# Performance work log

Measured on AMD Instinct MI355X. Metric: run time of the kernel, lower is better.

The kernel has to match this reference:

```python
import jax, jax.numpy as jnp
import numpy as np

B, T, NODES, D = 8, 32, 400, 64   # batch graphs, time steps, stocks, node_feat_dim==lstm_dim
N = B * T * NODES                 # 102400 total nodes
E = 1_638_400                     # edges (avg degree 16)
L1, L2, FC1, FC2 = 96, 64, 128, 3

def setup_inputs() -> dict:
    key = jax.random.key(0)
    ks = jax.random.split(key, 12)
    rn = lambda k, shape, s=0.05: jax.random.normal(k, shape, jnp.float32) * s
    return {
        "x": jax.random.normal(ks[0], (N, D), jnp.float32),
        "edge_attr": jax.random.normal(ks[1], (E, 2), jnp.float32),
        "conv1_w": rn(ks[2], (D, L1)), "conv1_b": jnp.zeros((L1,), jnp.float32),
        "conv2_w": rn(ks[3], (L1, L2)), "conv2_b": jnp.zeros((L2,), jnp.float32),
        "lstm_w_ih": rn(ks[4], (4 * D, D)), "lstm_w_hh": rn(ks[5], (4 * D, D)),
        "lstm_b_ih": jnp.zeros((4 * D,), jnp.float32), "lstm_b_hh": jnp.zeros((4 * D,), jnp.float32),
        "fc1_w": rn(ks[6], (FC1, L2)), "fc1_b": jnp.zeros((FC1,), jnp.float32),
        "fc2_w": rn(ks[7], (FC2, FC1)), "fc2_b": jnp.zeros((FC2,), jnp.float32),
        "edge_index": jax.random.randint(ks[8], (2, E), 0, N, jnp.int32),
    }

def _normalize(x):
    m = x.mean(axis=0, keepdims=True)
    s = x.std(axis=0, ddof=1, keepdims=True)  # torch.std uses ddof=1
    return (x - m) / s

def _gcn(x, W, b, src, dst, ew):
    """GCNConv with edge weights: add self-loops (weight 1), symmetric norm, scatter-add."""
    n = x.shape[0]
    loops = jnp.arange(n, dtype=src.dtype)
    src2 = jnp.concatenate([src, loops])
    dst2 = jnp.concatenate([dst, loops])
    ew2 = jnp.concatenate([ew, jnp.ones((n,), ew.dtype)])
    deg = jax.ops.segment_sum(ew2, dst2, num_segments=n)
    dis = jnp.where(deg > 0, jax.lax.rsqrt(jnp.where(deg > 0, deg, 1.0)), 0.0)
    norm = dis[src2] * ew2 * dis[dst2]
    h = x @ W                                        # [N, out]
    return jax.ops.segment_sum(h[src2] * norm[:, None], dst2, num_segments=n) + b

def _lstm_last(xseq, w_ih, w_hh, b_ih, b_hh):
    """Single-layer LSTM (torch gate order i,f,g,o); returns last hidden state."""
    Bn = xseq.shape[0]
    H = w_hh.shape[1]
    xg = jnp.einsum('btd,gd->tbg', xseq, w_ih) + (b_ih + b_hh)  # [T, Bn, 4H]
    def step(carry, g_in):
        h, c = carry
        g = g_in + h @ w_hh.T
        i, f, gg, o = jnp.split(g, 4, axis=-1)
        c = jax.nn.sigmoid(f) * c + jax.nn.sigmoid(i) * jnp.tanh(gg)
        h = jax.nn.sigmoid(o) * jnp.tanh(c)
        return (h, c), None
    init = (jnp.zeros((Bn, H), xseq.dtype), jnp.zeros((Bn, H), xseq.dtype))
    (h, _), _ = jax.lax.scan(step, init, xg)
    return h

def reference(x, edge_attr, conv1_w, conv1_b, conv2_w, conv2_b,
              lstm_w_ih, lstm_w_hh, lstm_b_ih, lstm_b_hh,
              fc1_w, fc1_b, fc2_w, fc2_b, edge_index):
    xn = _normalize(x)
    ew = jnp.abs(edge_attr[:, 0])        # args.edgetype = 0
    src, dst = edge_index[0], edge_index[1]
    # (first LSTM over raw x in the original is dead code: output immediately overwritten)
    h = jax.nn.relu(_gcn(xn, conv1_w, conv1_b, src, dst, ew))
    h = jax.nn.relu(_gcn(h, conv2_w, conv2_b, src, dst, ew))
    # to_dense_batch (batch-contiguous nodes) + reshape/permute into per-node time series
    h = h.reshape(B, T, NODES, L2).transpose(0, 2, 1, 3).reshape(B * NODES, T, L2)
    h = _lstm_last(h, lstm_w_ih, lstm_w_hh, lstm_b_ih, lstm_b_hh)   # [B*NODES, L2]
    h = jax.nn.relu(h @ fc1_w.T + fc1_b)
    logits = h @ fc2_w.T + fc2_b
    p = jax.nn.softmax(logits, axis=1)   # softmax over class dim of 2D tensor
    return p.reshape(B, NODES, FC2)
```

## Files before the change

kernel.cpp:

```cpp
#include <hip/hip_runtime.h>
#include <hip/hip_bf16.h>
#include <hip/hip_fp16.h>

#define NN 102400
#define DD 64
#define EE 1638400
#define L1C 96
#define L2C 64
#define TT 32
#define NODESC 400
#define BB 8
#define SS 3200
#define G4 256

#define NBUK 400
#define BCAP 5120
#define PCHUNK 2048
#define NPART (EE / PCHUNK)
#define PTHR 512
#define EPT (PCHUNK / PTHR)

#define OFF_ENT  ((size_t)0)
#define OFF_A1   ((size_t)4096000)
#define OFF_G1   ((size_t)10649600)
#define OFF_ENT2 ((size_t)26214400)
#define OFF_H2   ((size_t)26214400)
#define OFF_G2   ((size_t)32768000)
#define OFF_GCUR ((size_t)39321600)
#define OFF_DIS  ((size_t)39328000)
#define OFF_RNG  ((size_t)39430400)
#define OFF_HL   ((size_t)39635200)
#define OFF_ST   ((size_t)39840000)

typedef __attribute__((ext_vector_type(8))) _Float16 f16x8;
typedef __attribute__((ext_vector_type(4))) float f32x4;

__device__ __forceinline__ void fma4(float4& a, float s, const float4& w) {
    a.x = fmaf(s, w.x, a.x); a.y = fmaf(s, w.y, a.y);
    a.z = fmaf(s, w.z, a.z); a.w = fmaf(s, w.w, a.w);
}
__device__ __forceinline__ float rcp_f(float x) { return __builtin_amdgcn_rcpf(x); }
__device__ __forceinline__ float sigm_f(float x) {
    x = fminf(fmaxf(x, -30.f), 30.f);
    return rcp_f(1.f + __expf(-x));
}
__device__ __forceinline__ float tanh_f(float x) {
    x = fminf(fmaxf(x, -15.f), 15.f);
    float e = __expf(2.f * x);
    return (e - 1.f) * rcp_f(e + 1.f);
}
__device__ __forceinline__ unsigned short f32_bf16_rtne(float f) {
    unsigned int u = __float_as_uint(f);
    unsigned int r = u + 0x7fffu + ((u >> 16) & 1u);
    return (unsigned short)(r >> 16);
}
__device__ __forceinline__ float bf16_f32(unsigned short h) {
    return __uint_as_float(((unsigned int)h) << 16);
}
__device__ __forceinline__ float4 unp4(uint2 p) {
    float4 v;
    v.x = __uint_as_float(p.x << 16);
    v.y = __uint_as_float(p.x & 0xffff0000u);
    v.z = __uint_as_float(p.y << 16);
    v.w = __uint_as_float(p.y & 0xffff0000u);
    return v;
}
__device__ __forceinline__ uint2 pk4(float4 v) {
    unsigned int u0 = ((unsigned int)f32_bf16_rtne(v.y) << 16) | f32_bf16_rtne(v.x);
    unsigned int u1 = ((unsigned int)f32_bf16_rtne(v.w) << 16) | f32_bf16_rtne(v.z);
    return make_uint2(u0, u1);
}
__device__ __forceinline__ uint2 pkh4(float4 v) {
    __half2 h0 = __floats2half2_rn(v.x, v.y);
    __half2 h1 = __floats2half2_rn(v.z, v.w);
    uint2 r;
    r.x = *(unsigned int*)&h0;
    r.y = *(unsigned int*)&h1;
    return r;
}
__device__ __forceinline__ float4 uph4(uint2 p) {
    __half2 h0 = *(__half2*)&p.x;
    __half2 h1 = *(__half2*)&p.y;
    float2 f0 = __half22float2(h0), f1 = __half22float2(h1);
    return make_float4(f0.x, f0.y, f1.x, f1.y);
}

__global__ void init_zero(int* gcur, float* st) {
    int idx = blockIdx.x * 256 + threadIdx.x;
    if (idx < NBUK * 16) gcur[idx] = 0;
    if (blockIdx.x == 0 && threadIdx.x < 128) st[threadIdx.x] = 0.f;
}

__global__ __launch_bounds__(256) void col_sums(const float* __restrict__ x, float* __restrict__ st) {
    int c = threadIdx.x & 63;
    size_t i = (size_t)blockIdx.x * 256 + threadIdx.x;
    size_t stride = (size_t)gridDim.x * 256;
    float s = 0.f, q = 0.f;
    for (size_t e = i; e < (size_t)NN * 64; e += stride) {
        float v = x[e]; s += v; q = fmaf(v, v, q);
    }
    __shared__ float ls[128];
    if (threadIdx.x < 128) ls[threadIdx.x] = 0.f;
    __syncthreads();
    atomicAdd(&ls[c], s); atomicAdd(&ls[64 + c], q);
    __syncthreads();
    if (threadIdx.x < 128) atomicAdd(&st[threadIdx.x], ls[threadIdx.x]);
}

__global__ void finalize_stats(float* st) {
    int c = threadIdx.x;
    if (c < 64) {
        float s = st[c], q = st[64 + c];
        float mean = s / (float)NN;
        float var = (q - s * s / (float)NN) / (float)(NN - 1);
        st[128 + c] = mean;
        st[192 + c] = rsqrtf(fmaxf(var, 1e-20f));
    }
}

__global__ __launch_bounds__(256) void xnd_kernel(const float* __restrict__ x, const float* __restrict__ st,
                                                  const float* __restrict__ dis, uint2* __restrict__ xnd) {
    size_t i = (size_t)blockIdx.x * 256 + threadIdx.x;
    int n = (int)(i >> 4), q = (int)(i & 15);
    float4 v = ((const float4*)x)[i];
    float4 mean4 = ((const float4*)(st + 128))[q];
    float4 istd4 = ((const float4*)(st + 192))[q];
    float dn = dis[n];
    v.x = (v.x - mean4.x) * istd4.x * dn;
    v.y = (v.y - mean4.y) * istd4.y * dn;
    v.z = (v.z - mean4.z) * istd4.z * dn;
    v.w = (v.w - mean4.w) * istd4.w * dn;
    xnd[i] = pk4(v);
}

__global__ __launch_bounds__(PTHR) void part_kernel(const int* __restrict__ ei, const float* __restrict__ ea,
                                                    int* __restrict__ gcur, int2* __restrict__ ent2) {
    __shared__ int lhist[NBUK];
    __shared__ int lofs[NBUK];
    __shared__ int lbase[NBUK];
    __shared__ int scn[PTHR];
    __shared__ int2 stage[PCHUNK];
    __shared__ int  gdst[PCHUNK];
    const int tid = threadIdx.x;
    const int e0 = blockIdx.x * PCHUNK;
    for (int i = tid; i < NBUK; i += PTHR) lhist[i] = 0;
    __syncthreads();
    int   dv[EPT]; int sv[EPT]; float wvv[EPT];
    #pragma unroll
    for (int i = 0; i < EPT; ++i) {
        int e = e0 + i * PTHR + tid;
        dv[i]  = ei[EE + e];
        sv[i]  = ei[e];
        wvv[i] = fabsf(ea[2 * (size_t)e]);
        atomicAdd(&lhist[dv[i] >> 8], 1);
    }
    __syncthreads();
    scn[tid] = (tid < NBUK) ? lhist[tid] : 0;
    __syncthreads();
    for (int d = 1; d < PTHR; d <<= 1) {
        int t = (tid >= d) ? scn[tid - d] : 0;
        __syncthreads();
        scn[tid] += t;
        __syncthreads();
    }
    if (tid < NBUK) {
        lofs[tid]  = scn[tid] - lhist[tid];
        lbase[tid] = atomicAdd(&gcur[tid * 16], lhist[tid]);
        lhist[tid] = 0;
    }
    __syncthreads();
    #pragma unroll
    for (int i = 0; i < EPT; ++i) {
        int d = dv[i];
        int b = d >> 8;
        int li = atomicAdd(&lhist[b], 1);
        int pos = lofs[b] + li;
        stage[pos] = make_int2(sv[i] | ((d & 255) << 24), __float_as_int(wvv[i]));
        int gp_ = lbase[b] + li;
        gdst[pos] = (gp_ < BCAP) ? (b * BCAP + gp_) : -1;
    }
    __syncthreads();
    for (int i = tid; i < PCHUNK; i += PTHR) {
        int g = gdst[i];
        if (g >= 0) ent2[g] = stage[i];
    }
}

__global__ __launch_bounds__(256) void bucket_csr(const int2* __restrict__ ent2, const int* __restrict__ gcur,
                                                  int2* __restrict__ ent, int2* __restrict__ rng,
                                                  float* __restrict__ dis) {
    __shared__ int nhist[256];
    __shared__ int scn[256];
    __shared__ float wsum[256];
    __shared__ int pcur[256];
    const int tid = threadIdx.x;
    const int b = blockIdx.x;
    const int base = b * BCAP;
    int cnt = gcur[b * 16];
    if (cnt > BCAP) cnt = BCAP;
    nhist[tid] = 0;
    wsum[tid] = 0.f;
    __syncthreads();
    for (int e = tid; e < cnt; e += 256) {
        int2 en = ent2[base + e];
        int dl = ((unsigned)en.x) >> 24;
        atomicAdd(&nhist[dl], 1);
        atomicAdd(&wsum[dl], __int_as_float(en.y));
    }
    __syncthreads();
    int c = nhist[tid];
    scn[tid] = c;
    __syncthreads();
    for (int d = 1; d < 256; d <<= 1) {
        int t = (tid >= d) ? scn[tid - d] : 0;
        __syncthreads();
        scn[tid] += t;
        __syncthreads();
    }
    int ps = scn[tid] - c;
    rng[b * 256 + tid] = make_int2(base + ps, base + ps + c);
    dis[b * 256 + tid] = rsqrtf(1.f + wsum[tid]);
    pcur[tid] = ps;
    __syncthreads();
    for (int e = tid; e < cnt; e += 256) {
        int2 en = ent2[base + e];
        int dl = ((unsigned)en.x) >> 24;
        int local = atomicAdd(&pcur[dl], 1);
        ent[base + local] = make_int2(en.x & 0xFFFFFF, en.y);
    }
}

template<int K, int NC, int MB, int THREADS, bool PRELU, bool DISO, bool HIN, bool HOUT>
__global__ __launch_bounds__(THREADS) void gemm_tiled(
    const float* __restrict__ A, const float* __restrict__ Wm,
    const float* __restrict__ bin, const float* __restrict__ dscale,
    float* __restrict__ Cm, int ldC)
{
    __shared__ float As[MB * K];
    __shared__ float Ws[K * NC];

    for (int i = threadIdx.x; i < K * NC / 4; i += THREADS)
        ((float4*)Ws)[i] = ((const float4*)Wm)[i];

    size_t row0 = (size_t)blockIdx.x * MB;
    for (int i = threadIdx.x; i < MB * (K / 4); i += THREADS) {
        int r = i / (K / 4); int c = (i % (K / 4)) * 4;
        float4 a;
        if (HIN) {
            uint2 p = *(const uint2*)((const unsigned short*)A + (row0 + r) * K + c);
            a = uph4(p);
        } else {
            a = *(const float4*)(A + (row0 + r) * K + c);
        }
        if (PRELU) {
            a.x = fmaxf(a.x + bin[c + 0], 0.f); a.y = fmaxf(a.y + bin[c + 1], 0.f);
            a.z = fmaxf(a.z + bin[c + 2], 0.f); a.w = fmaxf(a.w + bin[c + 3], 0.f);
        }
        ((float4*)As)[i] = a;
    }
    __syncthreads();

    constexpr int NCT = NC / 4;
    int tc = threadIdx.x % NCT;
    int tr = threadIdx.x / NCT;
    int r = tr * 4;
    float4 acc[4];
    acc[0] = acc[1] = acc[2] = acc[3] = make_float4(0.f, 0.f, 0.f, 0.f);

    #pragma unroll 8
    for (int d4 = 0; d4 < K / 4; ++d4) {
        float4 w0 = ((const float4*)Ws)[(4 * d4 + 0) * NCT + tc];
        float4 w1 = ((const float4*)Ws)[(4 * d4 + 1) * NCT + tc];
        float4 w2 = ((const float4*)Ws)[(4 * d4 + 2) * NCT + tc];
        float4 w3 = ((const float4*)Ws)[(4 * d4 + 3) * NCT + tc];
        #pragma unroll
        for (int i = 0; i < 4; ++i) {
            float4 av = ((const float4*)As)[(r + i) * (K / 4) + d4];
            fma4(acc[i], av.x, w0); fma4(acc[i], av.y, w1);
            fma4(acc[i], av.z, w2); fma4(acc[i], av.w, w3);
        }
    }

    #pragma unroll
    for (int i = 0; i < 4; ++i) {
        size_t row = row0 + r + i;
        float4 o = acc[i];
        if (DISO) {
            float dn = dscale[row];
            o.x *= dn; o.y *= dn; o.z *= dn; o.w *= dn;
            *(uint2*)((unsigned short*)Cm + row * ldC + tc * 4) = pk4(o);
        } else if (HOUT) {
            *(uint2*)((unsigned short*)Cm + row * ldC + tc * 4) = pkh4(o);
        } else {
            *(float4*)(Cm + row * ldC + tc * 4) = o;
        }
    }
}

template<int C4>
__global__ __launch_bounds__(256) void gcn_gather(const uint2* __restrict__ h, const int2* __restrict__ rng,
                                                  const int2* __restrict__ ent, const float* __restrict__ dis,
                                                  unsigned short* __restrict__ g) {
    unsigned int idx = blockIdx.x * 256 + threadIdx.x;
    unsigned int n = idx / C4, q = idx % C4;
    float4 acc = unp4(h[(size_t)n * C4 + q]);
    int2 r = rng[n];
    int e = r.x;
    for (; e + 8 <= r.y; e += 8) {
        int2 en0 = ent[e],     en1 = ent[e + 1], en2 = ent[e + 2], en3 = ent[e + 3];
        int2 en4 = ent[e + 4], en5 = ent[e + 5], en6 = ent[e + 6], en7 = ent[e + 7];
        uint2 v0 = h[(size_t)en0.x * C4 + q];
        uint2 v1 = h[(size_t)en1.x * C4 + q];
        uint2 v2 = h[(size_t)en2.x * C4 + q];
        uint2 v3 = h[(size_t)en3.x * C4 + q];
        uint2 v4 = h[(size_t)en4.x * C4 + q];
        uint2 v5 = h[(size_t)en5.x * C4 + q];
        uint2 v6 = h[(size_t)en6.x * C4 + q];
        uint2 v7 = h[(size_t)en7.x * C4 + q];
        fma4(acc, __int_as_float(en0.y), unp4(v0));
        fma4(acc, __int_as_float(en1.y), unp4(v1));
        fma4(acc, __int_as_float(en2.y), unp4(v2));
        fma4(acc, __int_as_float(en3.y), unp4(v3));
        fma4(acc, __int_as_float(en4.y), unp4(v4));
        fma4(acc, __int_as_float(en5.y), unp4(v5));
        fma4(acc, __int_as_float(en6.y), unp4(v6));
        fma4(acc, __int_as_float(en7.y), unp4(v7));
    }
    for (; e + 4 <= r.y; e += 4) {
        int2 en0 = ent[e], en1 = ent[e + 1], en2 = ent[e + 2], en3 = ent[e + 3];
        uint2 v0 = h[(size_t)en0.x * C4 + q];
        uint2 v1 = h[(size_t)en1.x * C4 + q];
        uint2 v2 = h[(size_t)en2.x * C4 + q];
        uint2 v3 = h[(size_t)en3.x * C4 + q];
        fma4(acc, __int_as_float(en0.y), unp4(v0));
        fma4(acc, __int_as_float(en1.y), unp4(v1));
        fma4(acc, __int_as_float(en2.y), unp4(v2));
        fma4(acc, __int_as_float(en3.y), unp4(v3));
    }
    for (; e < r.y; ++e) {
        int2 en = ent[e];
        uint2 v = h[(size_t)en.x * C4 + q];
        fma4(acc, __int_as_float(en.y), unp4(v));
    }
    float dn = dis[n];
    acc.x *= dn; acc.y *= dn; acc.z *= dn; acc.w *= dn;
    *(uint2*)(g + (size_t)n * (C4 * 4) + q * 4) = pkh4(acc);
}

#define XP_LD 72
#define HP_LD2 72
#define GP_LD 258

__global__ __launch_bounds__(512, 1) void lstm_kernel(
    const __half* __restrict__ g2, const float* __restrict__ cb2,
    const float* __restrict__ whh, const float* __restrict__ wih,
    const float* __restrict__ bih, const float* __restrict__ bhh,
    float* __restrict__ hlast)
{
    __shared__ __align__(16) _Float16 xpack[32 * 16 * XP_LD];
    __shared__ __align__(16) _Float16 hhi[16 * HP_LD2];
    __shared__ __align__(16) _Float16 hlo[16 * HP_LD2];
    __shared__ float gp[16 * GP_LD];
    const int tid  = threadIdx.x;
    const int lane = tid & 63;
    const int wv   = tid >> 6;
    const int n15  = lane & 15;
    const int quad = lane >> 4;
    const int ja   = lane;

    f16x8 whh_h[2][2], whh_l[2][2], wih_h[2][2], wih_l[2][2];
    #pragma unroll
    for (int tl = 0; tl < 2; ++tl) {
        const int gate = (wv + 8 * tl) * 16 + n15;
        const float* wp = whh + (size_t)gate * 64 + quad * 8;
        const float* xp = wih + (size_t)gate * 64 + quad * 8;
        #pragma unroll
        for (int kc = 0; kc < 2; ++kc) {
            #pragma unroll
            for (int j = 0; j < 8; ++j) {
                float w = wp[kc * 32 + j];
                _Float16 h = (_Float16)w;
                whh_h[tl][kc][j] = h;
                whh_l[tl][kc][j] = (_Float16)((w - (float)h) * 2048.f);
                float v = xp[kc * 32 + j];
                _Float16 g = (_Float16)v;
                wih_h[tl][kc][j] = g;
                wih_l[tl][kc][j] = (_Float16)((v - (float)g) * 2048.f);
            }
        }
    }

    const float bi_i = bih[ja]        + bhh[ja];
    const float bi_f = bih[64 + ja]   + bhh[64 + ja];
    const float bi_g = bih[128 + ja]  + bhh[128 + ja];
    const float bi_o = bih[192 + ja]  + bhh[192 + ja];

    {
        const int s0 = blockIdx.x * 16;
        const int b_ = s0 / NODESC;
        const int node0 = s0 - b_ * NODESC;
        const int r  = (tid >> 4) & 15;
        const int c4 = tid & 15;
        const int t0 = tid >> 8;
        float4 bias4 = *(const float4*)(cb2 + c4 * 4);
        _Float16* dst = xpack + r * XP_LD + c4 * 4;
        const __half* src = g2 + ((size_t)(b_ * TT + t0) * NODESC + node0 + r) * 64 + c4 * 4;
        #pragma unroll
        for (int i = 0; i < 16; ++i) {
            uint2 p = *(const uint2*)(src + (size_t)i * 2 * NODESC * 64);
            float4 v = uph4(p);
            v.x = fmaxf(v.x + bias4.x, 0.f);
            v.y = fmaxf(v.y + bias4.y, 0.f);
            v.z = fmaxf(v.z + bias4.z, 0.f);
            v.w = fmaxf(v.w + bias4.w, 0.f);
            *(uint2*)(dst + (size_t)(t0 + i * 2) * (16 * XP_LD)) = pkh4(v);
        }
    }

    for (int i = tid; i < 16 * HP_LD2; i += 512) { hhi[i] = (_Float16)0.f; hlo[i] = (_Float16)0.f; }
    float cA_reg = 0.f, hA = 0.f;
    float cB_reg = 0.f, hB = 0.f;
    __syncthreads();

    const int xbase = n15 * XP_LD + quad * 8;
    const int hbase = n15 * HP_LD2 + quad * 8;

    for (int t = 0; t < TT; ++t) {
        f32x4 cmA  = {0.f,0.f,0.f,0.f}, clA0 = {0.f,0.f,0.f,0.f}, clA1 = {0.f,0.f,0.f,0.f};
        f32x4 cmB  = {0.f,0.f,0.f,0.f}, clB0 = {0.f,0.f,0.f,0.f}, clB1 = {0.f,0.f,0.f,0.f};
        const _Float16* xrow = xpack + (size_t)t * (16 * XP_LD);
        {
            f16x8 ax0 = *(const f16x8*)(xrow + xbase);
            f16x8 ah0 = *(const f16x8*)(hhi + hbase);
            f16x8 al0 = *(const f16x8*)(hlo + hbase);
            f16x8 ax1 = *(const f16x8*)(xrow + xbase + 32);
            f16x8 ah1 = *(const f16x8*)(hhi + hbase + 32);
            f16x8 al1 = *(const f16x8*)(hlo + hbase + 32);
            cmA  = __builtin_amdgcn_mfma_f32_16x16x32_f16(ax0, wih_h[0][0], cmA,  0, 0, 0);
            cmB  = __builtin_amdgcn_mfma_f32_16x16x32_f16(ax0, wih_h[1][0], cmB,  0, 0, 0);
            clA0 = __builtin_amdgcn_mfma_f32_16x16x32_f16(ax0, wih_l[0][0], clA0, 0, 0, 0);
            clB0 = __builtin_amdgcn_mfma_f32_16x16x32_f16(ax0, wih_l[1][0], clB0, 0, 0, 0);
            clA1 = __builtin_amdgcn_mfma_f32_16x16x32_f16(ax1, wih_l[0][1], clA1, 0, 0, 0);
            clB1 = __builtin_amdgcn_mfma_f32_16x16x32_f16(ax1, wih_l[1][1], clB1, 0, 0, 0);
            cmA  = __builtin_amdgcn_mfma_f32_16x16x32_f16(ah0, whh_h[0][0], cmA,  0, 0, 0);
            cmB  = __builtin_amdgcn_mfma_f32_16x16x32_f16(ah0, whh_h[1][0], cmB,  0, 0, 0);
            clA0 = __builtin_amdgcn_mfma_f32_16x16x32_f16(al0, whh_h[0][0], clA0, 0, 0, 0);
            clB0 = __builtin_amdgcn_mfma_f32_16x16x32_f16(al0, whh_h[1][0], clB0, 0, 0, 0);
            clA1 = __builtin_amdgcn_mfma_f32_16x16x32_f16(al1, whh_h[0][1], clA1, 0, 0, 0);
            clB1 = __builtin_amdgcn_mfma_f32_16x16x32_f16(al1, whh_h[1][1], clB1, 0, 0, 0);
            cmA  = __builtin_amdgcn_mfma_f32_16x16x32_f16(ax1, wih_h[0][1], cmA,  0, 0, 0);
            cmB  = __builtin_amdgcn_mfma_f32_16x16x32_f16(ax1, wih_h[1][1], cmB,  0, 0, 0);
            clA0 = __builtin_amdgcn_mfma_f32_16x16x32_f16(ah0, whh_l[0][0], clA0, 0, 0, 0);
            clB0 = __builtin_amdgcn_mfma_f32_16x16x32_f16(ah0, whh_l[1][0], clB0, 0, 0, 0);
            clA1 = __builtin_amdgcn_mfma_f32_16x16x32_f16(ah1, whh_l[0][1], clA1, 0, 0, 0);
            clB1 = __builtin_amdgcn_mfma_f32_16x16x32_f16(ah1, whh_l[1][1], clB1, 0, 0, 0);
            cmA  = __builtin_amdgcn_mfma_f32_16x16x32_f16(ah1, whh_h[0][1], cmA,  0, 0, 0);
            cmB  = __builtin_amdgcn_mfma_f32_16x16x32_f16(ah1, whh_h[1][1], cmB,  0, 0, 0);
        }
        f32x4 cA = cmA + (clA0 + clA1) * (1.f / 2048.f);
        f32x4 cB = cmB + (clB0 + clB1) * (1.f / 2048.f);
        #pragma unroll
        for (int r = 0; r < 4; ++r) {
            gp[(quad * 4 + r) * GP_LD + wv * 16 + n15]       = cA[r];
            gp[(quad * 4 + r) * GP_LD + (wv + 8) * 16 + n15] = cB[r];
        }
        __syncthreads();

        {
            const int qa = wv;
            float gi = gp[qa * GP_LD + ja]        + bi_i;
            float gf = gp[qa * GP_LD + 64 + ja]   + bi_f;
            float gg = gp[qa * GP_LD + 128 + ja]  + bi_g;
            float go = gp[qa * GP_LD + 192 + ja]  + bi_o;
            cA_reg = sigm_f(gf) * cA_reg + sigm_f(gi) * tanh_f(gg);
            hA = sigm_f(go) * tanh_f(cA_reg);
            _Float16 hh = (_Float16)hA;
            hhi[qa * HP_LD2 + ja] = hh;
            hlo[qa * HP_LD2 + ja] = (_Float16)((hA - (float)hh) * 2048.f);
        }
        {
            const int qa = wv + 8;
            float gi = gp[qa * GP_LD + ja]        + bi_i;
            float gf = gp[qa * GP_LD + 64 + ja]   + bi_f;
            float gg = gp[qa * GP_LD + 128 + ja]  + bi_g;
            float go = gp[qa * GP_LD + 192 + ja]  + bi_o;
            cB_reg = sigm_f(gf) * cB_reg + sigm_f(gi) * tanh_f(gg);
            hB = sigm_f(go) * tanh_f(cB_reg);
            _Float16 hh = (_Float16)hB;
            hhi[qa * HP_LD2 + ja] = hh;
            hlo[qa * HP_LD2 + ja] = (_Float16)((hB - (float)hh) * 2048.f);
        }
        __syncthreads();
    }
    hlast[((size_t)blockIdx.x * 16 + wv) * 64 + ja]     = hA;
    hlast[((size_t)blockIdx.x * 16 + wv + 8) * 64 + ja] = hB;
}

__global__ __launch_bounds__(128) void head_kernel(const float* __restrict__ hl,
                                                   const float* __restrict__ w1, const float* __restrict__ b1,
                                                   const float* __restrict__ w2, const float* __restrict__ b2,
                                                   float* __restrict__ out) {
    __shared__ float hrow[64];
    __shared__ float a1[128];
    __shared__ float lg[3];
    int s = blockIdx.x, tid = threadIdx.x;
    if (tid < 64) hrow[tid] = hl[(size_t)s * 64 + tid];
    __syncthreads();
    {
        const float4* wr = (const float4*)(w1 + (size_t)tid * 64);
        const float4* hq = (const float4*)hrow;
        float4 acc = make_float4(0.f, 0.f, 0.f, 0.f);
        #pragma unroll
        for (int k = 0; k < 16; ++k) {
            float4 wv = wr[k]; float4 hv = hq[k];
            acc.x = fmaf(wv.x, hv.x, acc.x); acc.y = fmaf(wv.y, hv.y, acc.y);
            acc.z = fmaf(wv.z, hv.z, acc.z); acc.w = fmaf(wv.w, hv.w, acc.w);
        }
        a1[tid] = fmaxf((acc.x + acc.y) + (acc.z + acc.w) + b1[tid], 0.f);
    }
    __syncthreads();
    if (tid < 3) {
        const float4* wr = (const float4*)(w2 + (size_t)tid * 128);
        const float4* aq = (const float4*)a1;
        float4 acc = make_float4(0.f, 0.f, 0.f, 0.f);
        #pragma unroll
        for (int k = 0; k < 32; ++k) {
            float4 wv = wr[k]; float4 av = aq[k];
            acc.x = fmaf(wv.x, av.x, acc.x); acc.y = fmaf(wv.y, av.y, acc.y);
            acc.z = fmaf(wv.z, av.z, acc.z); acc.w = fmaf(wv.w, av.w, acc.w);
        }
        lg[tid] = (acc.x + acc.y) + (acc.z + acc.w) + b2[tid];
    }
    __syncthreads();
    if (tid == 0) {
        float m = fmaxf(lg[0], fmaxf(lg[1], lg[2]));
        float e0 = __expf(lg[0] - m), e1 = __expf(lg[1] - m), e2 = __expf(lg[2] - m);
        float inv = 1.f / (e0 + e1 + e2);
        out[(size_t)s * 3 + 0] = e0 * inv;
        out[(size_t)s * 3 + 1] = e1 * inv;
        out[(size_t)s * 3 + 2] = e2 * inv;
    }
}

extern "C" void kernel_launch(void* const* d_in, const int* in_sizes, int n_in,
                              void* d_out, int out_size, void* d_ws, size_t ws_size,
                              hipStream_t stream) {
    (void)in_sizes; (void)n_in; (void)out_size; (void)ws_size;
    const float* x        = (const float*)d_in[0];
    const float* ea       = (const float*)d_in[1];
    const float* conv1_w  = (const float*)d_in[2];
    const float* conv1_b  = (const float*)d_in[3];
    const float* conv2_w  = (const float*)d_in[4];
    const float* conv2_b  = (const float*)d_in[5];
    const float* w_ih     = (const float*)d_in[6];
    const float* w_hh     = (const float*)d_in[7];
    const float* b_ih     = (const float*)d_in[8];
    const float* b_hh     = (const float*)d_in[9];
    const float* fc1_w    = (const float*)d_in[10];
    const float* fc1_b    = (const float*)d_in[11];
    const float* fc2_w    = (const float*)d_in[12];
    const float* fc2_b    = (const float*)d_in[13];
    const int*   ei       = (const int*)d_in[14];
    float* out = (float*)d_out;

    float* W    = (float*)d_ws;
    int2*  ent  = (int2*)(W + OFF_ENT);
    unsigned short* a1h = (unsigned short*)(W + OFF_A1);
    unsigned short* g1h = (unsigned short*)(W + OFF_G1);
    int2*  ent2 = (int2*)(W + OFF_ENT2);
    uint2* xnd  = (uint2*)(W + OFF_ENT2);
    float* h2   = W + OFF_H2;
    unsigned short* g2h = (unsigned short*)(W + OFF_G2);
    int*   gcur = (int*)(W + OFF_GCUR);
    float* dis  = W + OFF_DIS;
    int2*  rng  = (int2*)(W + OFF_RNG);
    float* hl   = W + OFF_HL;
    float* st   = W + OFF_ST;

    init_zero<<<26, 256, 0, stream>>>(gcur, st);
    col_sums<<<1024, 256, 0, stream>>>(x, st);
    finalize_stats<<<1, 64, 0, stream>>>(st);

    part_kernel<<<NPART, PTHR, 0, stream>>>(ei, ea, gcur, ent2);
    bucket_csr<<<NBUK, 256, 0, stream>>>(ent2, gcur, ent, rng, dis);

    xnd_kernel<<<NN * 16 / 256, 256, 0, stream>>>(x, st, dis, xnd);

    gcn_gather<16><<<NN * 16 / 256, 256, 0, stream>>>(xnd, rng, ent, dis, a1h);
    gemm_tiled<64, 96, 32, 192, false, false, true, true><<<NN / 32, 192, 0, stream>>>(
        (const float*)a1h, conv1_w, nullptr, nullptr, (float*)g1h, 96);

    gemm_tiled<96, 64, 64, 256, true, true, true, false><<<NN / 64, 256, 0, stream>>>(
        (const float*)g1h, conv2_w, conv1_b, dis, h2, 64);
    gcn_gather<16><<<NN * 16 / 256, 256, 0, stream>>>((const uint2*)h2, rng, ent, dis, g2h);

    lstm_kernel<<<SS / 16, 512, 0, stream>>>((const __half*)g2h, conv2_b, w_hh, w_ih,
                                             b_ih, b_hh, hl);

    head_kernel<<<SS, 128, 0, stream>>>(hl, fc1_w, fc1_b, fc2_w, fc2_b, out);
}
```

Before: 376.5 us.

## Replace FP32 tiled GEMMs for both GCN layers with split-FP16 MFMA kernels

Swaps the two scalar FP32 shared-memory GEMMs for MFMA 16x16x32 f16 kernels. The weights are split into a high FP16 part and a scaled low FP16 residual so that FP32-like accuracy is kept with two MFMAs per tile. Each wave holds its weight fragments in registers, and the A tiles are staged in padded LDS. The second GEMM keeps the bias+ReLU prologue and the degree-scale epilogue, writing bf16. This aims to cut the ALU-bound GEMM time, at the cost of a small precision change and scattered 2-byte output stores.

```diff
diff --git a/kernel.cpp b/kernel.cpp
--- a/kernel.cpp
+++ b/kernel.cpp
@@ -230,69 +230,142 @@
     }
 }
 
-template<int K, int NC, int MB, int THREADS, bool PRELU, bool DISO, bool HIN, bool HOUT>
-__global__ __launch_bounds__(THREADS) void gemm_tiled(
-    const float* __restrict__ A, const float* __restrict__ Wm,
-    const float* __restrict__ bin, const float* __restrict__ dscale,
-    float* __restrict__ Cm, int ldC)
-{
-    __shared__ float As[MB * K];
-    __shared__ float Ws[K * NC];
-
-    for (int i = threadIdx.x; i < K * NC / 4; i += THREADS)
-        ((float4*)Ws)[i] = ((const float4*)Wm)[i];
-
-    size_t row0 = (size_t)blockIdx.x * MB;
-    for (int i = threadIdx.x; i < MB * (K / 4); i += THREADS) {
-        int r = i / (K / 4); int c = (i % (K / 4)) * 4;
-        float4 a;
-        if (HIN) {
-            uint2 p = *(const uint2*)((const unsigned short*)A + (row0 + r) * K + c);
-            a = uph4(p);
-        } else {
-            a = *(const float4*)(A + (row0 + r) * K + c);
-        }
-        if (PRELU) {
-            a.x = fmaxf(a.x + bin[c + 0], 0.f); a.y = fmaxf(a.y + bin[c + 1], 0.f);
-            a.z = fmaxf(a.z + bin[c + 2], 0.f); a.w = fmaxf(a.w + bin[c + 3], 0.f);
-        }
-        ((float4*)As)[i] = a;
-    }
-    __syncthreads();
-
-    constexpr int NCT = NC / 4;
-    int tc = threadIdx.x % NCT;
-    int tr = threadIdx.x / NCT;
-    int r = tr * 4;
-    float4 acc[4];
-    acc[0] = acc[1] = acc[2] = acc[3] = make_float4(0.f, 0.f, 0.f, 0.f);
-
-    #pragma unroll 8
-    for (int d4 = 0; d4 < K / 4; ++d4) {
-        float4 w0 = ((const float4*)Ws)[(4 * d4 + 0) * NCT + tc];
-        float4 w1 = ((const float4*)Ws)[(4 * d4 + 1) * NCT + tc];
-        float4 w2 = ((const float4*)Ws)[(4 * d4 + 2) * NCT + tc];
-        float4 w3 = ((const float4*)Ws)[(4 * d4 + 3) * NCT + tc];
-        #pragma unroll
-        for (int i = 0; i < 4; ++i) {
-            float4 av = ((const float4*)As)[(r + i) * (K / 4) + d4];
-            fma4(acc[i], av.x, w0); fma4(acc[i], av.y, w1);
-            fma4(acc[i], av.z, w2); fma4(acc[i], av.w, w3);
-        }
-    }
-
-    #pragma unroll
-    for (int i = 0; i < 4; ++i) {
-        size_t row = row0 + r + i;
-        float4 o = acc[i];
-        if (DISO) {
-            float dn = dscale[row];
-            o.x *= dn; o.y *= dn; o.z *= dn; o.w *= dn;
-            *(uint2*)((unsigned short*)Cm + row * ldC + tc * 4) = pk4(o);
-        } else if (HOUT) {
-            *(uint2*)((unsigned short*)Cm + row * ldC + tc * 4) = pkh4(o);
-        } else {
-            *(float4*)(Cm + row * ldC + tc * 4) = o;
+#define G1_LD 72
+__global__ __launch_bounds__(192) void gemm1_mfma(const unsigned short* __restrict__ A,
+                                                  const float* __restrict__ Wm,
+                                                  unsigned short* __restrict__ Cm) {
+    __shared__ __align__(16) _Float16 As[64 * G1_LD];
+    const int tid  = threadIdx.x;
+    const int lane = tid & 63;
+    const int wv   = tid >> 6;
+    const int n15  = lane & 15;
+    const int quad = lane >> 4;
+    const size_t row0 = (size_t)blockIdx.x * 64;
+
+    f16x8 wh[2][2], wl[2][2];
+    #pragma unroll
+    for (int t = 0; t < 2; ++t) {
+        const int col = (wv + 3 * t) * 16 + n15;
+        #pragma unroll
+        for (int kc = 0; kc < 2; ++kc) {
+            #pragma unroll
+            for (int j = 0; j < 8; ++j) {
+                float w = Wm[(size_t)(kc * 32 + quad * 8 + j) * 96 + col];
+                _Float16 h = (_Float16)w;
+                wh[t][kc][j] = h;
+                wl[t][kc][j] = (_Float16)((w - (float)h) * 2048.f);
+            }
+        }
+    }
+
+    for (int i = tid; i < 64 * 16; i += 192) {
+        int r = i >> 4, c4 = i & 15;
+        uint2 p = *(const uint2*)(A + (row0 + r) * 64 + c4 * 4);
+        *(uint2*)(As + r * G1_LD + c4 * 4) = p;
+    }
+    __syncthreads();
+
+    f32x4 acc[2][4], accl[2][4];
+    #pragma unroll
+    for (int t = 0; t < 2; ++t)
+        #pragma unroll
+        for (int rt = 0; rt < 4; ++rt) {
+            acc[t][rt]  = (f32x4){0.f, 0.f, 0.f, 0.f};
+            accl[t][rt] = (f32x4){0.f, 0.f, 0.f, 0.f};
+        }
+    #pragma unroll
+    for (int kc = 0; kc < 2; ++kc) {
+        #pragma unroll
+        for (int rt = 0; rt < 4; ++rt) {
+            f16x8 a = *(const f16x8*)(As + (rt * 16 + n15) * G1_LD + kc * 32 + quad * 8);
+            #pragma unroll
+            for (int t = 0; t < 2; ++t) {
+                acc[t][rt]  = __builtin_amdgcn_mfma_f32_16x16x32_f16(a, wh[t][kc], acc[t][rt],  0, 0, 0);
+                accl[t][rt] = __builtin_amdgcn_mfma_f32_16x16x32_f16(a, wl[t][kc], accl[t][rt], 0, 0, 0);
+            }
+        }
+    }
+    #pragma unroll
+    for (int t = 0; t < 2; ++t) {
+        const int col = (wv + 3 * t) * 16 + n15;
+        #pragma unroll
+        for (int rt = 0; rt < 4; ++rt) {
+            f32x4 c = acc[t][rt] + accl[t][rt] * (1.f / 2048.f);
+            #pragma unroll
+            for (int r = 0; r < 4; ++r) {
+                size_t row = row0 + rt * 16 + quad * 4 + r;
+                ((_Float16*)Cm)[row * 96 + col] = (_Float16)c[r];
+            }
+        }
+    }
+}
+
+#define G2_LD 104
+__global__ __launch_bounds__(256) void gemm2_mfma(const unsigned short* __restrict__ A,
+                                                  const float* __restrict__ Wm,
+                                                  const float* __restrict__ bin,
+                                                  const float* __restrict__ dscale,
+                                                  unsigned short* __restrict__ Cm) {
+    __shared__ __align__(16) _Float16 As[64 * G2_LD];
+    __shared__ float ds[64];
+    const int tid  = threadIdx.x;
+    const int lane = tid & 63;
+    const int wv   = tid >> 6;
+    const int n15  = lane & 15;
+    const int quad = lane >> 4;
+    const size_t row0 = (size_t)blockIdx.x * 64;
+
+    f16x8 wh[3], wl[3];
+    {
+        const int col = wv * 16 + n15;
+        #pragma unroll
+        for (int kc = 0; kc < 3; ++kc) {
+            #pragma unroll
+            for (int j = 0; j < 8; ++j) {
+                float w = Wm[(size_t)(kc * 32 + quad * 8 + j) * 64 + col];
+                _Float16 h = (_Float16)w;
+                wh[kc][j] = h;
+                wl[kc][j] = (_Float16)((w - (float)h) * 2048.f);
+            }
+        }
+    }
+    if (tid < 64) ds[tid] = dscale[row0 + tid];
+
+    for (int i = tid; i < 64 * 24; i += 256) {
+        int r = i / 24, c4 = i % 24;
+        uint2 p = *(const uint2*)(A + (row0 + r) * 96 + c4 * 4);
+        float4 v = uph4(p);
+        float4 b = *(const float4*)(bin + c4 * 4);
+        v.x = fmaxf(v.x + b.x, 0.f); v.y = fmaxf(v.y + b.y, 0.f);
+        v.z = fmaxf(v.z + b.z, 0.f); v.w = fmaxf(v.w + b.w, 0.f);
+        *(uint2*)(As + r * G2_LD + c4 * 4) = pkh4(v);
+    }
+    __syncthreads();
+
+    f32x4 acc[4], accl[4];
+    #pragma unroll
+    for (int rt = 0; rt < 4; ++rt) {
+        acc[rt]  = (f32x4){0.f, 0.f, 0.f, 0.f};
+        accl[rt] = (f32x4){0.f, 0.f, 0.f, 0.f};
+    }
+    #pragma unroll
+    for (int kc = 0; kc < 3; ++kc) {
+        #pragma unroll
+        for (int rt = 0; rt < 4; ++rt) {
+            f16x8 a = *(const f16x8*)(As + (rt * 16 + n15) * G2_LD + kc * 32 + quad * 8);
+            acc[rt]  = __builtin_amdgcn_mfma_f32_16x16x32_f16(a, wh[kc], acc[rt],  0, 0, 0);
+            accl[rt] = __builtin_amdgcn_mfma_f32_16x16x32_f16(a, wl[kc], accl[rt], 0, 0, 0);
+        }
+    }
+    const int col = wv * 16 + n15;
+    #pragma unroll
+    for (int rt = 0; rt < 4; ++rt) {
+        f32x4 c = acc[rt] + accl[rt] * (1.f / 2048.f);
+        #pragma unroll
+        for (int r = 0; r < 4; ++r) {
+            int row = rt * 16 + quad * 4 + r;
+            float v = c[r] * ds[row];
+            Cm[(row0 + row) * 64 + col] = f32_bf16_rtne(v);
         }
     }
 }
@@ -587,11 +660,9 @@
     xnd_kernel<<<NN * 16 / 256, 256, 0, stream>>>(x, st, dis, xnd);
 
     gcn_gather<16><<<NN * 16 / 256, 256, 0, stream>>>(xnd, rng, ent, dis, a1h);
-    gemm_tiled<64, 96, 32, 192, false, false, true, true><<<NN / 32, 192, 0, stream>>>(
-        (const float*)a1h, conv1_w, nullptr, nullptr, (float*)g1h, 96);
-
-    gemm_tiled<96, 64, 64, 256, true, true, true, false><<<NN / 64, 256, 0, stream>>>(
-        (const float*)g1h, conv2_w, conv1_b, dis, h2, 64);
+    gemm1_mfma<<<NN / 64, 192, 0, stream>>>(a1h, conv1_w, g1h);
+
+    gemm2_mfma<<<NN / 64, 256, 0, stream>>>(g1h, conv2_w, conv1_b, dis, (unsigned short*)h2);
     gcn_gather<16><<<NN * 16 / 256, 256, 0, stream>>>((const uint2*)h2, rng, ent, dis, g2h);
 
     lstm_kernel<<<SS / 16, 512, 0, stream>>>((const __half*)g2h, conv2_b, w_hh, w_ih,
```

Result: faster. 342.2 us (-9.1%).
